# Kernel optimization log

Hardware: AMD Instinct MI355X
Metric: run time of the kernel (lower is better)

The kernel has to match this reference:

```python
import jax, jax.numpy as jnp
import numpy as np

BETA = 1.0
POWER_ITERS = 9
EPS = 1e-12  # F.normalize default eps


def _normalize(v):
    # L2 normalize over dim=1 of [B, N, 1], matching F.normalize(x, dim=1)
    n = jnp.linalg.norm(v, axis=1, keepdims=True)
    return v / jnp.maximum(n, EPS)


def _dominant_eigenvalue(A, x):
    # A: [B, N, N], x: [B, N, 1]
    for _ in range(POWER_ITERS):
        x = _normalize(jnp.matmul(A, x))
    Ax = jnp.matmul(A, x)[..., 0]              # [B, N]
    num = jnp.sum(Ax * x[..., 0], axis=1)      # x^T A x
    den = jnp.sum(x[..., 0] ** 2, axis=1)      # ||x||^2 (== 1 after normalize)
    return num / den, x


def setup_inputs() -> dict:
    key = jax.random.key(0)
    k1, k2 = jax.random.split(key)
    B, C, H, W = 256, 2048, 7, 7
    x = jax.random.normal(k1, (B, C, H, W), dtype=jnp.float32)
    x0 = _normalize(jax.random.normal(k2, (B, H * W, 1), dtype=jnp.float32))
    return {"x": x, "x0": x0}


def reference(x, x0):
    B, C, H, W = x.shape
    N = H * W
    Wm = x.reshape(B, C, N)
    # ATA = W^T W : [B, N, N]
    ATA = jnp.einsum('bcn,bcm->bnm', Wm, Wm)
    # first power iteration: largest eigenvalue; x0 is a no_grad constant
    largest, x1 = _dominant_eigenvalue(ATA, jax.lax.stop_gradient(x0))
    I = jnp.eye(N, dtype=ATA.dtype)
    shifted = ATA - largest[:, None, None] * I
    # second power iteration warm-started from detached x1 (torch stores last_x detached)
    tmp, _ = _dominant_eigenvalue(shifted, jax.lax.stop_gradient(x1))
    smallest = tmp + largest
    penalty = BETA * (largest / smallest - 1.0) ** 2
    return jnp.sum(penalty) / B
```

## Files before the change

kernel.cpp:

```cpp
#include <hip/hip_runtime.h>
#include <hip/hip_bf16.h>
#include <stdint.h>


#define BATCH 256
#define CDIM  2048
#define NDIM  49
#define HALF_K 1024
#define CHUNK 128
#define CHUNK_FLOATS (CHUNK * NDIM)
#define CHUNK_F4 (CHUNK_FLOATS / 4)
#define NPAD 64
#define ASTRIDE 53

typedef __bf16 bf16x8 __attribute__((ext_vector_type(8)));
typedef float  f32x16 __attribute__((ext_vector_type(16)));

__device__ inline void async_load16(const float* g, float* l) {
  __builtin_amdgcn_global_load_lds(
      (const __attribute__((address_space(1))) void*)g,
      (__attribute__((address_space(3))) void*)l,
      16 , 0 , 0 );
}

__global__ __launch_bounds__(256) void gram_kernel(
    const float* __restrict__ x, float* __restrict__ partial) {
  __shared__ float raw[CHUNK_FLOATS + 16];

  const int tid  = threadIdx.x;
  const int bidx = blockIdx.x;
  const int batch = bidx >> 1;
  const int lane = tid & 63;
  const int wv   = tid >> 6;
  const int ln   = lane & 31;
  const int hf   = lane >> 5;
  const int qm   = wv >> 1, qn = wv & 1;
  const int m = qm * 32 + ln;
  const int n = qn * 32 + ln;

  const float* gbase = x + (size_t)batch * (CDIM * NDIM)
                         + (size_t)(bidx & 1) * (HALF_K * NDIM);

  f32x16 c1, c2, c3;
#pragma unroll
  for (int i = 0; i < 16; ++i) { c1[i] = 0.f; c2[i] = 0.f; c3[i] = 0.f; }

  for (int ch = 0; ch < HALF_K / CHUNK; ++ch) {
    __syncthreads();
    const float* gch = gbase + ch * CHUNK_FLOATS;
#pragma unroll
    for (int i = 0; i < (CHUNK_F4 + 255) / 256; ++i) {
      int slot = i * 256 + tid;
      if (slot < CHUNK_F4) async_load16(gch + slot * 4, &raw[slot * 4]);
    }
    __syncthreads();

#pragma unroll
    for (int s = 0; s < CHUNK / 16; ++s) {
      const int kk = s * 16 + hf * 8;
      const float* pa = &raw[kk * NDIM + m];
      const float* pb = &raw[kk * NDIM + n];
      bf16x8 ah, al, bh, bl;
#pragma unroll
      for (int j = 0; j < 8; ++j) {
        float av = pa[j * NDIM];
        __bf16 h = (__bf16)av;
        ah[j] = h;
        al[j] = (__bf16)(av - (float)h);
        float bv = pb[j * NDIM];
        __bf16 hb = (__bf16)bv;
        bh[j] = hb;
        bl[j] = (__bf16)(bv - (float)hb);
      }
      c1 = __builtin_amdgcn_mfma_f32_32x32x16_bf16(ah, bh, c1, 0, 0, 0);
      c2 = __builtin_amdgcn_mfma_f32_32x32x16_bf16(ah, bl, c2, 0, 0, 0);
      c3 = __builtin_amdgcn_mfma_f32_32x32x16_bf16(al, bh, c3, 0, 0, 0);
    }
  }

  float* out = partial + (size_t)bidx * (NPAD * NPAD);
#pragma unroll
  for (int r = 0; r < 16; ++r) {
    int row = (r & 3) + 8 * (r >> 2) + 4 * hf;
    int mm = qm * 32 + row;
    if (mm < NDIM && n < NDIM)
      out[mm * NPAD + n] = c1[r] + c2[r] + c3[r];
  }
}

__global__ __launch_bounds__(64) void eigen_kernel(
    const float* __restrict__ partial, const float* __restrict__ x0,
    float* __restrict__ out) {
  __shared__ float A[NDIM * ASTRIDE];
  __shared__ float xv[64];

  const int b = blockIdx.x;
  const int t = threadIdx.x;
  const float* p0 = partial + (size_t)(2 * b) * (NPAD * NPAD);
  const float* p1 = p0 + NPAD * NPAD;

  for (int idx = t; idx < NDIM * NDIM; idx += 64) {
    int r = idx / NDIM;
    int c = idx - r * NDIM;
    A[r * ASTRIDE + c] = p0[r * NPAD + c] + p1[r * NPAD + c];
  }
  if (t < NDIM) xv[t] = x0[b * NDIM + t];
  __syncthreads();

  auto rayleigh_power = [&](float shift) -> float {
    for (int it = 0; it < 9; ++it) {
      float y = 0.f;
      if (t < NDIM) {
        const float* Ar = &A[t * ASTRIDE];
#pragma unroll 7
        for (int k = 0; k < NDIM; ++k) y = fmaf(Ar[k], xv[k], y);
        y -= shift * xv[t];
      }
      float s = y * y;
#pragma unroll
      for (int o = 32; o; o >>= 1) s += __shfl_xor(s, o, 64);
      float nrm = fmaxf(sqrtf(s), 1e-12f);
      __syncthreads();
      if (t < NDIM) xv[t] = y / nrm;
      __syncthreads();
    }
    float yy = 0.f;
    if (t < NDIM) {
      const float* Ar = &A[t * ASTRIDE];
#pragma unroll 7
      for (int k = 0; k < NDIM; ++k) yy = fmaf(Ar[k], xv[k], yy);
      yy -= shift * xv[t];
    }
    float num = (t < NDIM) ? yy * xv[t] : 0.f;
    float den = (t < NDIM) ? xv[t] * xv[t] : 0.f;
#pragma unroll
    for (int o = 32; o; o >>= 1) {
      num += __shfl_xor(num, o, 64);
      den += __shfl_xor(den, o, 64);
    }
    return num / den;
  };

  float largest = rayleigh_power(0.f);
  float tmp = rayleigh_power(largest);
  float smallest = tmp + largest;

  if (t == 0) {
    float r = largest / smallest - 1.f;
    atomicAdd(out, r * r * (1.0f / (float)BATCH));
  }
}

extern "C" void kernel_launch(void* const* d_in, const int* in_sizes, int n_in,
                              void* d_out, int out_size, void* d_ws,
                              size_t ws_size, hipStream_t stream) {
  const float* x  = (const float*)d_in[0];
  const float* x0 = (const float*)d_in[1];
  float* out = (float*)d_out;
  float* partial = (float*)d_ws;

  hipMemsetAsync(d_out, 0, sizeof(float), stream);
  gram_kernel<<<512, 256, 0, stream>>>(x, partial);
  eigen_kernel<<<BATCH, 64, 0, stream>>>(partial, x0, out);
}
```

Before: 182.4 us.

## Double-buffer gram chunks, split K four ways, fold memset into kernel

The gram kernel now splits each batch's channel dimension into four quarters (1024 blocks instead of 512) and double-buffers smaller 64-channel chunks, so the next chunk's async load overlaps the MFMA work on the current one. Partial results are stored densely as 49x49, and the eigen kernel sums four partials instead of two. The separate memset launch is replaced by the first thread of the gram kernel zeroing the output. Costs are more partial-sum traffic, a higher occupancy request in launch bounds, and the ordering of that zero-write against the eigen kernel's atomics relies on the two kernels running in sequence on the same stream.

```diff
diff --git a/kernel.cpp b/kernel.cpp
--- a/kernel.cpp
+++ b/kernel.cpp
@@ -6,11 +6,14 @@
 #define BATCH 256
 #define CDIM  2048
 #define NDIM  49
-#define HALF_K 1024
-#define CHUNK 128
+#define QK    512
+#define NQ    4
+#define CHUNK 64
+#define NCHUNK (QK / CHUNK)
 #define CHUNK_FLOATS (CHUNK * NDIM)
 #define CHUNK_F4 (CHUNK_FLOATS / 4)
-#define NPAD 64
+#define CPAD (CHUNK_FLOATS + 16)
+#define PSIZE (NDIM * NDIM)
 #define ASTRIDE 53
 
 typedef __bf16 bf16x8 __attribute__((ext_vector_type(8)));
@@ -23,13 +26,15 @@
       16 , 0 , 0 );
 }
 
-__global__ __launch_bounds__(256) void gram_kernel(
-    const float* __restrict__ x, float* __restrict__ partial) {
-  __shared__ float raw[CHUNK_FLOATS + 16];
+__global__ __launch_bounds__(256, 4) void gram_kernel(
+    const float* __restrict__ x, float* __restrict__ partial,
+    float* __restrict__ out) {
+  __shared__ float raw[2][CPAD];
 
   const int tid  = threadIdx.x;
   const int bidx = blockIdx.x;
-  const int batch = bidx >> 1;
+  const int batch = bidx >> 2;
+  const int q     = bidx & 3;
   const int lane = tid & 63;
   const int wv   = tid >> 6;
   const int ln   = lane & 31;
@@ -38,28 +43,40 @@
   const int m = qm * 32 + ln;
   const int n = qn * 32 + ln;
 
+  if (bidx == 0 && tid == 0) out[0] = 0.f;
+
   const float* gbase = x + (size_t)batch * (CDIM * NDIM)
-                         + (size_t)(bidx & 1) * (HALF_K * NDIM);
+                         + (size_t)q * (QK * NDIM);
 
   f32x16 c1, c2, c3;
 #pragma unroll
   for (int i = 0; i < 16; ++i) { c1[i] = 0.f; c2[i] = 0.f; c3[i] = 0.f; }
 
-  for (int ch = 0; ch < HALF_K / CHUNK; ++ch) {
+#pragma unroll
+  for (int i = 0; i < (CHUNK_F4 + 255) / 256; ++i) {
+    int slot = i * 256 + tid;
+    if (slot < CHUNK_F4) async_load16(gbase + slot * 4, &raw[0][slot * 4]);
+  }
+
+  for (int ch = 0; ch < NCHUNK; ++ch) {
     __syncthreads();
-    const float* gch = gbase + ch * CHUNK_FLOATS;
+    const int cur = ch & 1;
+    if (ch + 1 < NCHUNK) {
+      const float* gch = gbase + (ch + 1) * CHUNK_FLOATS;
+      float* dst = raw[cur ^ 1];
 #pragma unroll
-    for (int i = 0; i < (CHUNK_F4 + 255) / 256; ++i) {
-      int slot = i * 256 + tid;
-      if (slot < CHUNK_F4) async_load16(gch + slot * 4, &raw[slot * 4]);
+      for (int i = 0; i < (CHUNK_F4 + 255) / 256; ++i) {
+        int slot = i * 256 + tid;
+        if (slot < CHUNK_F4) async_load16(gch + slot * 4, &dst[slot * 4]);
+      }
     }
-    __syncthreads();
 
+    const float* buf = raw[cur];
 #pragma unroll
     for (int s = 0; s < CHUNK / 16; ++s) {
       const int kk = s * 16 + hf * 8;
-      const float* pa = &raw[kk * NDIM + m];
-      const float* pb = &raw[kk * NDIM + n];
+      const float* pa = &buf[kk * NDIM + m];
+      const float* pb = &buf[kk * NDIM + n];
       bf16x8 ah, al, bh, bl;
 #pragma unroll
       for (int j = 0; j < 8; ++j) {
@@ -78,13 +95,13 @@
     }
   }
 
-  float* out = partial + (size_t)bidx * (NPAD * NPAD);
+  float* outp = partial + (size_t)bidx * PSIZE;
 #pragma unroll
   for (int r = 0; r < 16; ++r) {
     int row = (r & 3) + 8 * (r >> 2) + 4 * hf;
     int mm = qm * 32 + row;
     if (mm < NDIM && n < NDIM)
-      out[mm * NPAD + n] = c1[r] + c2[r] + c3[r];
+      outp[mm * NDIM + n] = c1[r] + c2[r] + c3[r];
   }
 }
 
@@ -96,13 +113,15 @@
 
   const int b = blockIdx.x;
   const int t = threadIdx.x;
-  const float* p0 = partial + (size_t)(2 * b) * (NPAD * NPAD);
-  const float* p1 = p0 + NPAD * NPAD;
+  const float* p0 = partial + (size_t)(NQ * b) * PSIZE;
 
   for (int idx = t; idx < NDIM * NDIM; idx += 64) {
     int r = idx / NDIM;
     int c = idx - r * NDIM;
-    A[r * ASTRIDE + c] = p0[r * NPAD + c] + p1[r * NPAD + c];
+    float v = 0.f;
+#pragma unroll
+    for (int qq = 0; qq < NQ; ++qq) v += p0[qq * PSIZE + idx];
+    A[r * ASTRIDE + c] = v;
   }
   if (t < NDIM) xv[t] = x0[b * NDIM + t];
   __syncthreads();
@@ -159,7 +178,6 @@
   float* out = (float*)d_out;
   float* partial = (float*)d_ws;
 
-  hipMemsetAsync(d_out, 0, sizeof(float), stream);
-  gram_kernel<<<512, 256, 0, stream>>>(x, partial);
+  gram_kernel<<<1024, 256, 0, stream>>>(x, partial, out);
   eigen_kernel<<<BATCH, 64, 0, stream>>>(partial, x0, out);
 }
```

Result: faster. 177.7 us (-2.5%).
